# Kernel optimization log

Hardware: AMD Instinct MI355X
Metric: run time of the kernel (lower is better)

Reference implementation:

```python
import jax, jax.numpy as jnp
import numpy as np

B, M, NT, V, D, H, E, S = 4, 12, 12, 10000, 64, 3, 512, 32


def setup_inputs() -> dict:
    key = jax.random.key(0)
    ks = jax.random.split(key, 16)
    def rn(k, shape, scale=0.05):
        return jax.random.normal(k, shape, dtype=jnp.float32) * scale
    return {
        "tendency": jax.random.normal(ks[0], (B, M, V), dtype=jnp.float32),
        "periodicity": jax.random.normal(ks[1], (B, NT, V), dtype=jnp.float32),
        "edges": jax.random.randint(ks[2], (H, E, S), 0, V),
        "w1": rn(ks[3], (1, D)), "b1": rn(ks[4], (D,)),
        "w2": rn(ks[5], (D, D)), "b2": rn(ks[6], (D,)),
        "attn_w": rn(ks[7], (D, D)), "attn_a": rn(ks[8], (2 * D, 1)),
        "w_ih": rn(ks[9], (4 * D, D)), "w_hh": rn(ks[10], (4 * D, D)),
        "b_ih": rn(ks[11], (4 * D,)), "b_hh": rn(ks[12], (4 * D,)),
        "w_out": rn(ks[13], (2 * D, 1)), "b_out": rn(ks[14], (1,)),
    }


def _hypersage(X, edges, w, b):
    # X: (N, V, F); edges: (E, S) node indices. All edges have size S <= Q,
    # so torch's random subsampling is the identity.
    n, v, f = X.shape
    e, s = edges.shape
    gathered = X[:, edges, :]                      # (N, E, S, F)
    agg = gathered.mean(axis=2)                    # (N, E, F)
    flat = edges.reshape(-1)                       # (E*S,)
    contrib = jnp.broadcast_to(agg[:, :, None, :], (n, e, s, f)).reshape(n, e * s, f)
    X_out = jnp.zeros((n, v, f), X.dtype).at[:, flat, :].add(contrib)
    deg = jnp.zeros((v,), X.dtype).at[flat].add(1.0)
    deg = jnp.maximum(deg, 1.0)
    X_out = X_out / deg[None, :, None]
    return X_out @ w + b                           # Linear fc


def _attention(Xs, attn_w, attn_a):
    # Xs: (H, N, V, D)
    ref = Xs.mean(axis=0)                          # (N, V, D)
    wx = Xs @ attn_w                               # (H, N, V, D)
    wr = ref @ attn_w                              # (N, V, D)
    z = jnp.concatenate([wx, jnp.broadcast_to(wr[None], wx.shape)], axis=-1) @ attn_a
    z = jax.nn.leaky_relu(z, negative_slope=0.2)   # (H, N, V, 1)
    alpha = jax.nn.softmax(z, axis=0)
    return (alpha * Xs).sum(axis=0)                # (N, V, D)


def _lstm_final(x, w_ih, w_hh, b_ih, b_hh):
    # x: (BV, T, D) -> final hidden state (BV, D). PyTorch gate order i,f,g,o.
    bv, t, d = x.shape
    xg = x @ w_ih.T + (b_ih + b_hh)                # precompute input gates (BV, T, 4D)
    def step(carry, xg_t):
        h, c = carry
        g = xg_t + h @ w_hh.T
        i, f, gg, o = jnp.split(g, 4, axis=-1)
        c = jax.nn.sigmoid(f) * c + jax.nn.sigmoid(i) * jnp.tanh(gg)
        h = jax.nn.sigmoid(o) * jnp.tanh(c)
        return (h, c), None
    h0 = jnp.zeros((bv, d), x.dtype)
    (h, _), _ = jax.lax.scan(step, (h0, h0), jnp.swapaxes(xg, 0, 1))
    return h


def _branch(seq, edges, w1, b1, w2, b2, attn_w, attn_a, w_ih, w_hh, b_ih, b_hh):
    b, t, v = seq.shape
    X = seq.reshape(b * t, v, 1)                   # fold time into batch (same DAMHG per step)
    def per_hg(e):
        return _hypersage(_hypersage(X, e, w1, b1), e, w2, b2)
    xs = jax.vmap(per_hg)(edges)                   # (H, B*T, V, D)
    fused = _attention(xs, attn_w, attn_a)         # (B*T, V, D)
    d = fused.shape[-1]
    seq_v = fused.reshape(b, t, v, d).transpose(0, 2, 1, 3).reshape(b * v, t, d)
    h = _lstm_final(seq_v, w_ih, w_hh, b_ih, b_hh)
    return h.reshape(b, v, d)


def reference(tendency, periodicity, edges, w1, b1, w2, b2, attn_w, attn_a, w_ih, w_hh, b_ih, b_hh, w_out, b_out):
    h_t = _branch(tendency, edges, w1, b1, w2, b2, attn_w, attn_a, w_ih, w_hh, b_ih, b_hh)
    h_p = _branch(periodicity, edges, w1, b1, w2, b2, attn_w, attn_a, w_ih, w_hh, b_ih, b_hh)
    fusion = jnp.concatenate([h_t, h_p], axis=-1)  # (B, V, 2D)
    out = fusion @ w_out + b_out                   # (B, V, 1)
    return out[..., 0]
```

## Files before the change

kernel.cpp:

```cpp
#include <hip/hip_runtime.h>

#define NV 10000
#define NB 4
#define NTT 12
#define NSEQ 48
#define NH 3
#define NE 512
#define NS 32
#define ND 64

#define S_U   0
#define S_C1  64
#define S_V1  128
#define S_V2  192
#define S_SC  256
#define S_GU  272
#define S_GC  528
#define S_G0  784
#define F_INV 1040
#define F_M   (F_INV + NH*NV)
#define F_PQ  (F_M + NH*NV)
#define F_HT  (F_PQ + 4*NV*NSEQ)
#define I_CNT (F_HT + 2*NB*NV)
#define I_CUR (I_CNT + NH*NV)
#define I_OFF (I_CUR + NH*NV)
#define I_SLOT (I_OFF + NH*NV)
#define F_DYN (I_SLOT + NH*NE*NS)
#define XT_SZ  (NV*NSEQ)
#define AGG_SZ (NH*NE*NSEQ)
#define YZ_SZ  (NH*NV*NSEQ)

#define NZERO (2*NH*NV + NB*NV)

typedef __attribute__((ext_vector_type(8))) _Float16 f16x8;
typedef __attribute__((ext_vector_type(4))) float f32x4;

__device__ __forceinline__ unsigned short f2h(float x) {
  union { _Float16 h; unsigned short u; } c;
  c.h = (_Float16)x;
  return c.u;
}
__device__ __forceinline__ f16x8 ldsH(const unsigned short* p) {
  union { uint4 u; f16x8 v; } x;
  x.u = *(const uint4*)p;
  return x.v;
}

__global__ void k_init(const float* __restrict__ w1, const float* __restrict__ b1,
                       const float* __restrict__ w2, const float* __restrict__ b2,
                       const float* __restrict__ attn_w, const float* __restrict__ attn_a,
                       const float* __restrict__ w_ih, const float* __restrict__ b_ih,
                       const float* __restrict__ b_hh, float* __restrict__ ws,
                       int* __restrict__ cnt, float* __restrict__ out) {
  const int tid = threadIdx.x;
  if (blockIdx.x != 0) {
    const int g = (blockIdx.x - 1) * 256 + tid;
    if (g < 2 * NH * NV) cnt[g] = 0;
    else if (g < NZERO) out[g - 2 * NH * NV] = 0.0f;
    return;
  }
  __shared__ float u_s[64], c1_s[64];
  if (tid < 64) {
    float v1 = 0.f, v2 = 0.f, u = 0.f, c1 = 0.f;
    for (int d = 0; d < 64; ++d) {
      const float aw = attn_w[tid * 64 + d];
      v1 += aw * attn_a[d];
      v2 += aw * attn_a[64 + d];
      const float w2v = w2[d * 64 + tid];
      u  += w1[d] * w2v;
      c1 += b1[d] * w2v;
    }
    ws[S_U + tid] = u;  ws[S_C1 + tid] = c1;
    ws[S_V1 + tid] = v1; ws[S_V2 + tid] = v2;
    u_s[tid] = u; c1_s[tid] = c1;
  }
  __syncthreads();
  if (tid == 0) {
    float al = 0.f, be = 0.f, ga = 0.f, de = 0.f, ep = 0.f;
    for (int d = 0; d < 64; ++d) {
      const float v1 = ws[S_V1 + d], v2 = ws[S_V2 + d];
      al += u_s[d] * v1;  be += c1_s[d] * v1;
      ga += u_s[d] * v2;  de += c1_s[d] * v2;
      ep += b2[d] * (v1 + v2);
    }
    ws[S_SC + 0] = al; ws[S_SC + 1] = be; ws[S_SC + 2] = ga;
    ws[S_SC + 3] = de; ws[S_SC + 4] = ep;
  }
  {
    const int j = tid;
    float gu = 0.f, gc = 0.f, g0 = 0.f;
    for (int d = 0; d < 64; ++d) {
      const float w = w_ih[j * 64 + d];
      gu += w * u_s[d]; gc += w * c1_s[d]; g0 += w * b2[d];
    }
    ws[S_GU + j] = gu; ws[S_GC + j] = gc;
    ws[S_G0 + j] = g0 + b_ih[j] + b_hh[j];
  }
}

__global__ void k_count(const int* __restrict__ edges, int* __restrict__ counts) {
  const int g = blockIdx.x * 256 + threadIdx.x;
  if (g >= NH * NE * NS) return;
  const int h = g >> 14;
  atomicAdd(&counts[h * NV + edges[g]], 1);
}

__global__ void k_scan(const int* __restrict__ counts, int* __restrict__ offs,
                       float* __restrict__ invdeg, float* __restrict__ mvec) {
  const int h = blockIdx.x;
  const int tid = threadIdx.x;
  const int base = h * NV;
  const int CH = 10;
  int local[10];
  int run = 0;
  for (int i = 0; i < CH; ++i) {
    const int v = tid * CH + i;
    const int c = (v < NV) ? counts[base + v] : 0;
    local[i] = run; run += c;
  }
  __shared__ int sd[1024];
  sd[tid] = run;
  __syncthreads();
  int acc = run;
  for (int off = 1; off < 1024; off <<= 1) {
    const int t = (tid >= off) ? sd[tid - off] : 0;
    __syncthreads();
    acc += t; sd[tid] = acc;
    __syncthreads();
  }
  const int excl = acc - run;
  for (int i = 0; i < CH; ++i) {
    const int v = tid * CH + i;
    if (v < NV) {
      offs[base + v] = excl + local[i];
      const int c = counts[base + v];
      invdeg[base + v] = 1.0f / (float)((c > 0) ? c : 1);
      mvec[base + v] = (c > 0) ? 1.0f : 0.0f;
    }
  }
}

__global__ void k_fill(const int* __restrict__ edges, const int* __restrict__ offs,
                       int* __restrict__ cursor, int* __restrict__ slot_edge) {
  const int g = blockIdx.x * 256 + threadIdx.x;
  if (g >= NH * NE * NS) return;
  const int h = g >> 14;
  const int e = (g >> 5) & (NE - 1);
  const int v = edges[g];
  const int pos = atomicAdd(&cursor[h * NV + v], 1);
  slot_edge[h * NE * NS + offs[h * NV + v] + pos] = e;
}

__global__ void k_trans2(const float* __restrict__ s0, const float* __restrict__ s1,
                         float* __restrict__ xT, int xtS) {
  __shared__ float tile[128][49];
  const float* seq = blockIdx.y ? s1 : s0;
  float* o = xT + (size_t)blockIdx.y * xtS;
  const int v0 = blockIdx.x * 128;
  const int tid = threadIdx.x;
  for (int i = tid; i < 128 * NSEQ; i += 256) {
    const int n = i / 128, vl = i % 128;
    const int v = v0 + vl;
    tile[vl][n] = (v < NV) ? seq[n * NV + v] : 0.0f;
  }
  __syncthreads();
  for (int i = tid; i < 128 * NSEQ; i += 256) {
    const int vl = i / NSEQ, n = i % NSEQ;
    const int v = v0 + vl;
    if (v < NV) o[v * NSEQ + n] = tile[vl][n];
  }
}

__global__ void k_eagg1(const int* __restrict__ edges, const float* __restrict__ xT,
                        int xtS, float* __restrict__ agg, int aggS) {
  const int g = blockIdx.x * 256 + threadIdx.x;
  if (g >= NH * NE * 12) return;
  const float* x = xT + (size_t)blockIdx.y * xtS;
  float* a = agg + (size_t)blockIdx.y * aggS;
  const int n0 = (g % 12) * 4;
  const int e = (g / 12) % NE;
  const int h = g / (12 * NE);
  const int* ep = edges + (h * NE + e) * NS;
  float4 acc = make_float4(0.f, 0.f, 0.f, 0.f);
  for (int s = 0; s < NS; ++s) {
    const float4 t = *(const float4*)&x[ep[s] * NSEQ + n0];
    acc.x += t.x; acc.y += t.y; acc.z += t.z; acc.w += t.w;
  }
  acc.x *= (1.0f / NS); acc.y *= (1.0f / NS); acc.z *= (1.0f / NS); acc.w *= (1.0f / NS);
  *(float4*)&a[(h * NE + e) * NSEQ + n0] = acc;
}

__global__ void k_eagg2(const int* __restrict__ edges, const float* __restrict__ ysum,
                        int yS, const float* __restrict__ invdeg,
                        float* __restrict__ agg, int aggS) {
  const int g = blockIdx.x * 256 + threadIdx.x;
  if (g >= NH * NE * 12) return;
  const float* y = ysum + (size_t)blockIdx.y * yS;
  float* a = agg + (size_t)blockIdx.y * aggS;
  const int n0 = (g % 12) * 4;
  const int e = (g / 12) % NE;
  const int h = g / (12 * NE);
  const int* ep = edges + (h * NE + e) * NS;
  float4 acc = make_float4(0.f, 0.f, 0.f, 0.f);
  for (int s = 0; s < NS; ++s) {
    const int v = ep[s];
    const float iv = invdeg[h * NV + v];
    const float4 t = *(const float4*)&y[(h * NV + v) * NSEQ + n0];
    acc.x += t.x * iv; acc.y += t.y * iv; acc.z += t.z * iv; acc.w += t.w * iv;
  }
  acc.x *= (1.0f / NS); acc.y *= (1.0f / NS); acc.z *= (1.0f / NS); acc.w *= (1.0f / NS);
  *(float4*)&a[(h * NE + e) * NSEQ + n0] = acc;
}

__global__ void k_vg(const int* __restrict__ counts, const int* __restrict__ offs,
                     const int* __restrict__ slot_edge, const float* __restrict__ agg,
                     int aggS, float* __restrict__ outv, int outS) {
  const int g = blockIdx.x * 256 + threadIdx.x;
  if (g >= NH * NV * 12) return;
  const float* a = agg + (size_t)blockIdx.y * aggS;
  float* o = outv + (size_t)blockIdx.y * outS;
  const int n0 = (g % 12) * 4;
  const int v = (g / 12) % NV;
  const int h = g / (12 * NV);
  const int beg = offs[h * NV + v];
  const int cnt = counts[h * NV + v];
  const int* se = slot_edge + h * NE * NS;
  float4 acc = make_float4(0.f, 0.f, 0.f, 0.f);
  for (int i = 0; i < cnt; ++i) {
    const int e = se[beg + i];
    const float4 t = *(const float4*)&a[(h * NE + e) * NSEQ + n0];
    acc.x += t.x; acc.y += t.y; acc.z += t.z; acc.w += t.w;
  }
  *(float4*)&o[(h * NV + v) * NSEQ + n0] = acc;
}

__global__ void k_vgattn(const int* __restrict__ counts, const int* __restrict__ offs,
                         const int* __restrict__ slot_edge, const float* __restrict__ agg,
                         int aggS, const float* __restrict__ invdeg,
                         const float* __restrict__ mvec, const float* __restrict__ ws,
                         unsigned int* __restrict__ pq, int br0) {
  const int g = blockIdx.x * 256 + threadIdx.x;
  if (g >= NV * 12) return;
  const int bi = blockIdx.y;
  const float* a = agg + (size_t)bi * aggS;
  unsigned int* pbuf = pq + (size_t)(bi + br0) * NV * NSEQ;
  const int n0 = (g % 12) * 4;
  const int v = g / 12;
  const float al = ws[S_SC + 0], be = ws[S_SC + 1], ga = ws[S_SC + 2],
              de = ws[S_SC + 3], ep = ws[S_SC + 4];
  union { float4 v4; float f[4]; } zh[3];
  float mh[3];
  #pragma unroll
  for (int h = 0; h < NH; ++h) {
    const int beg = offs[h * NV + v];
    const int cnt = counts[h * NV + v];
    const int* se = slot_edge + h * NE * NS;
    float4 acc = make_float4(0.f, 0.f, 0.f, 0.f);
    for (int i = 0; i < cnt; ++i) {
      const int e = se[beg + i];
      const float4 t = *(const float4*)&a[(h * NE + e) * NSEQ + n0];
      acc.x += t.x; acc.y += t.y; acc.z += t.z; acc.w += t.w;
    }
    const float iv = invdeg[h * NV + v];
    zh[h].v4 = make_float4(acc.x * iv, acc.y * iv, acc.z * iv, acc.w * iv);
    mh[h] = mvec[h * NV + v];
  }
  const float mb = (mh[0] + mh[1] + mh[2]) * (1.f / 3.f);
  uint4 o4;
  unsigned int* op = (unsigned int*)&o4;
  #pragma unroll
  for (int j = 0; j < 4; ++j) {
    const float z0 = zh[0].f[j], z1 = zh[1].f[j], z2 = zh[2].f[j];
    const float zb = (z0 + z1 + z2) * (1.f / 3.f);
    float sc[3];
    const float zt[3] = {z0, z1, z2};
    #pragma unroll
    for (int h = 0; h < NH; ++h) {
      const float s = al * zt[h] + be * mh[h] + ga * zb + de * mb + ep;
      sc[h] = (s > 0.f) ? s : 0.2f * s;
    }
    const float mx = fmaxf(sc[0], fmaxf(sc[1], sc[2]));
    const float e0 = __expf(sc[0] - mx), e1 = __expf(sc[1] - mx), e2 = __expf(sc[2] - mx);
    const float inv = 1.0f / (e0 + e1 + e2);
    const float pv = (e0 * z0 + e1 * z1 + e2 * z2) * inv;
    const float qv = (e0 * mh[0] + e1 * mh[1] + e2 * mh[2]) * inv;
    op[j] = (unsigned int)f2h(pv) | ((unsigned int)f2h(qv) << 16);
  }
  *(uint4*)&pbuf[v * NSEQ + n0] = o4;
}

#define RS2 72
__launch_bounds__(256, 4)
__global__ void k_lstm2(const float* __restrict__ w_hh, const float* __restrict__ ws,
                        const unsigned int* __restrict__ pqbase,
                        const float* __restrict__ w_out, const float* __restrict__ b_out,
                        float* __restrict__ out) {
  __shared__ __align__(16) unsigned short smem[2 * 64 * RS2];
  __shared__ unsigned int pq_sh[NTT][64];
  const int tid = threadIdx.x;
  const int w = tid >> 6, lane = tid & 63, q = lane >> 4, l15 = lane & 15;
  const int b = blockIdx.y, br = blockIdx.z;
  const int v0 = blockIdx.x * 64;
  const int d = w * 16 + l15;

  union HU { uint4 u; f16x8 v; };

  const unsigned int* pqb = pqbase + (size_t)br * NV * NSEQ;
  if (tid < 192) {
    const int s = tid / 3, f4 = tid % 3;
    const int v = v0 + s;
    uint4 val = make_uint4(0u, 0u, 0u, 0u);
    if (v < NV) val = *(const uint4*)&pqb[v * NSEQ + b * NTT + f4 * 4];
    pq_sh[f4 * 4 + 0][s] = val.x; pq_sh[f4 * 4 + 1][s] = val.y;
    pq_sh[f4 * 4 + 2][s] = val.z; pq_sh[f4 * 4 + 3][s] = val.w;
  }

  f16x8 Bf[4][2];
  #pragma unroll
  for (int g = 0; g < 4; ++g)
    #pragma unroll
    for (int kh = 0; kh < 2; ++kh) {
      const float* wp = w_hh + (g * 64 + d) * 64 + kh * 32 + q * 8;
      const float4 lo = *(const float4*)wp;
      const float4 hi = *(const float4*)(wp + 4);
      HU f;
      f.u.x = (unsigned int)f2h(lo.x) | ((unsigned int)f2h(lo.y) << 16);
      f.u.y = (unsigned int)f2h(lo.z) | ((unsigned int)f2h(lo.w) << 16);
      f.u.z = (unsigned int)f2h(hi.x) | ((unsigned int)f2h(hi.y) << 16);
      f.u.w = (unsigned int)f2h(hi.z) | ((unsigned int)f2h(hi.w) << 16);
      Bf[g][kh] = f.v;
    }

  HU bex[4];
  #pragma unroll
  for (int g = 0; g < 4; ++g) {
    const float gu = ws[S_GU + g * 64 + d];
    const float gc = ws[S_GC + g * 64 + d];
    const float g0 = ws[S_G0 + g * 64 + d];
    bex[g].u.x = (q == 0) ? ((unsigned int)f2h(gu) | ((unsigned int)f2h(gc) << 16)) : 0u;
    bex[g].u.y = (q == 0) ? (unsigned int)f2h(g0) : 0u;
    bex[g].u.z = 0u; bex[g].u.w = 0u;
  }
  const float WO = w_out[br * 64 + d];
  const float BO = b_out[0];
  __syncthreads();

  f32x4 cst[4];
  float pr[4][4];
  #pragma unroll
  for (int mi = 0; mi < 4; ++mi) cst[mi] = (f32x4){0.f, 0.f, 0.f, 0.f};
  const f32x4 z4 = (f32x4){0.f, 0.f, 0.f, 0.f};

  #pragma unroll 1
  for (int t = 0; t < NTT; ++t) {
    const unsigned short* hr = smem + ((t + 1) & 1) * (64 * RS2);
    unsigned short* hw = smem + (t & 1) * (64 * RS2);
    const bool last = (t == NTT - 1);
    #pragma unroll
    for (int mi = 0; mi < 4; ++mi) {
      HU ae;
      ae.u.x = (q == 0) ? pq_sh[t][mi * 16 + l15] : 0u;
      ae.u.y = (q == 0) ? 0x3C00u : 0u;
      ae.u.z = 0u; ae.u.w = 0u;
      f32x4 aI = __builtin_amdgcn_mfma_f32_16x16x32_f16(ae.v, bex[0].v, z4, 0, 0, 0);
      f32x4 aF = __builtin_amdgcn_mfma_f32_16x16x32_f16(ae.v, bex[1].v, z4, 0, 0, 0);
      f32x4 aG = __builtin_amdgcn_mfma_f32_16x16x32_f16(ae.v, bex[2].v, z4, 0, 0, 0);
      f32x4 aO = __builtin_amdgcn_mfma_f32_16x16x32_f16(ae.v, bex[3].v, z4, 0, 0, 0);
      if (t > 0) {
        #pragma unroll
        for (int kh = 0; kh < 2; ++kh) {
          const f16x8 Ah = ldsH(&hr[(mi * 16 + l15) * RS2 + kh * 32 + q * 8]);
          aI = __builtin_amdgcn_mfma_f32_16x16x32_f16(Ah, Bf[0][kh], aI, 0, 0, 0);
          aF = __builtin_amdgcn_mfma_f32_16x16x32_f16(Ah, Bf[1][kh], aF, 0, 0, 0);
          aG = __builtin_amdgcn_mfma_f32_16x16x32_f16(Ah, Bf[2][kh], aG, 0, 0, 0);
          aO = __builtin_amdgcn_mfma_f32_16x16x32_f16(Ah, Bf[3][kh], aO, 0, 0, 0);
        }
      }
      #pragma unroll
      for (int r = 0; r < 4; ++r) {
        const float c  = cst[mi][r];
        const float ea = __expf(-aI[r]);
        const float eb = __expf(-2.0f * aG[r]);
        const float ef = __expf(-aF[r]);
        const float A  = 1.0f + ea, Bb = 1.0f + eb, Fd = 1.0f + ef;
        const float P  = A * Bb;
        const float numer = fmaf(c, P, (1.0f - eb) * Fd);
        const float cn = numer * __builtin_amdgcn_rcpf(Fd * P);
        cst[mi][r] = cn;
        const float ec = __expf(-aO[r]);
        const float ed = __expf(-2.0f * cn);
        const float h = (1.0f - ed) *
            __builtin_amdgcn_rcpf((1.0f + ec) * (1.0f + ed));
        if (!last) {
          hw[(mi * 16 + q * 4 + r) * RS2 + d] = f2h(h);
        } else {
          pr[mi][r] = h * WO;
        }
      }
    }
    __syncthreads();
  }
  float* fbuf = (float*)smem;
  #pragma unroll
  for (int mi = 0; mi < 4; ++mi)
    #pragma unroll
    for (int r = 0; r < 4; ++r) {
      float v = pr[mi][r];
      v += __shfl_xor(v, 1);
      v += __shfl_xor(v, 2);
      v += __shfl_xor(v, 4);
      v += __shfl_xor(v, 8);
      if (l15 == 0) fbuf[w * 64 + mi * 16 + q * 4 + r] = v;
    }
  __syncthreads();
  if (tid < 64) {
    const int v = v0 + tid;
    if (v < NV) {
      const float s = fbuf[tid] + fbuf[64 + tid] + fbuf[128 + tid] + fbuf[192 + tid];
      atomicAdd(&out[b * NV + v], s + ((br == 0) ? BO : 0.0f));
    }
  }
}

extern "C" void kernel_launch(void* const* d_in, const int* in_sizes, int n_in,
                              void* d_out, int out_size, void* d_ws, size_t ws_size,
                              hipStream_t stream) {
  const float* tend   = (const float*)d_in[0];
  const float* peri   = (const float*)d_in[1];
  const int*   edges  = (const int*)d_in[2];
  const float* w1     = (const float*)d_in[3];
  const float* b1     = (const float*)d_in[4];
  const float* w2     = (const float*)d_in[5];
  const float* b2     = (const float*)d_in[6];
  const float* attn_w = (const float*)d_in[7];
  const float* attn_a = (const float*)d_in[8];
  const float* w_ih   = (const float*)d_in[9];
  const float* w_hh   = (const float*)d_in[10];
  const float* b_ih   = (const float*)d_in[11];
  const float* b_hh   = (const float*)d_in[12];
  const float* w_out  = (const float*)d_in[13];
  const float* b_out  = (const float*)d_in[14];
  float* out = (float*)d_out;
  float* ws  = (float*)d_ws;
  int*   iws = (int*)d_ws;
  int* cnt = iws + I_CNT;
  int* cur = iws + I_CUR;
  int* off = iws + I_OFF;
  int* sed = iws + I_SLOT;
  unsigned int* pqw = (unsigned int*)(ws + F_PQ);

  const size_t need2 = ((size_t)F_DYN + 2 * (XT_SZ + AGG_SZ + YZ_SZ)) * 4;
  const bool batched = ws_size >= need2;
  const int nb = batched ? 2 : 1;
  float* XT  = ws + F_DYN;
  float* AGG = XT + (size_t)nb * XT_SZ;
  float* YZ  = AGG + (size_t)nb * AGG_SZ;

  k_init<<<1 + (NZERO + 255) / 256, 256, 0, stream>>>(
      w1, b1, w2, b2, attn_w, attn_a, w_ih, b_ih, b_hh, ws, cnt, out);
  k_count<<<(NH * NE * NS) / 256, 256, 0, stream>>>(edges, cnt);
  k_scan<<<NH, 1024, 0, stream>>>(cnt, off, ws + F_INV, ws + F_M);
  k_fill<<<(NH * NE * NS) / 256, 256, 0, stream>>>(edges, off, cur, sed);

  const int g_eagg = (NH * NE * 12 + 255) / 256;
  const int g_vg   = (NH * NV * 12 + 255) / 256;
  const int g_attn = (NV * 12 + 255) / 256;
  if (batched) {
    k_trans2<<<dim3((NV + 127) / 128, 2), 256, 0, stream>>>(tend, peri, XT, XT_SZ);
    k_eagg1<<<dim3(g_eagg, 2), 256, 0, stream>>>(edges, XT, XT_SZ, AGG, AGG_SZ);
    k_vg<<<dim3(g_vg, 2), 256, 0, stream>>>(cnt, off, sed, AGG, AGG_SZ, YZ, YZ_SZ);
    k_eagg2<<<dim3(g_eagg, 2), 256, 0, stream>>>(edges, YZ, YZ_SZ, ws + F_INV, AGG, AGG_SZ);
    k_vgattn<<<dim3(g_attn, 2), 256, 0, stream>>>(cnt, off, sed, AGG, AGG_SZ,
                                                  ws + F_INV, ws + F_M, ws, pqw, 0);
  } else {
    for (int br = 0; br < 2; ++br) {
      const float* seq = br ? peri : tend;
      k_trans2<<<dim3((NV + 127) / 128, 1), 256, 0, stream>>>(seq, seq, XT, 0);
      k_eagg1<<<dim3(g_eagg, 1), 256, 0, stream>>>(edges, XT, 0, AGG, 0);
      k_vg<<<dim3(g_vg, 1), 256, 0, stream>>>(cnt, off, sed, AGG, 0, YZ, 0);
      k_eagg2<<<dim3(g_eagg, 1), 256, 0, stream>>>(edges, YZ, 0, ws + F_INV, AGG, 0);
      k_vgattn<<<dim3(g_attn, 1), 256, 0, stream>>>(cnt, off, sed, AGG, 0,
                                                    ws + F_INV, ws + F_M, ws, pqw, br);
    }
  }
  dim3 lgrid((NV + 63) / 64, NB, 2);
  k_lstm2<<<lgrid, 256, 0, stream>>>(w_hh, ws, pqw, w_out, b_out, out);
}
```

Measured before the change: 242.9 us.

## Split edge aggregation across 8 lanes and halve LSTM vertex tile

The edge-aggregation kernels now spread each edge's 32 members across 8 lanes, each summing 4 gathered rows, and combine the partial sums with shuffle-xor reductions. This launches 8x more threads and exposes more memory-level parallelism for the scattered gathers. The LSTM kernel now processes 32 vertices per block instead of 64 on a flattened 1D grid, doubling block count to raise occupancy and cut tail effects. In exchange, each LSTM block loads its converted w_hh weights for half as many vertices, and half the MFMA tiles per wave are gone, so per-block fixed overhead grows.

New measurement: 238.1 us. -2.0%, faster.

```diff
diff --git a/kernel.cpp b/kernel.cpp
--- a/kernel.cpp
+++ b/kernel.cpp
@@ -8,6 +8,7 @@
 #define NE 512
 #define NS 32
 #define ND 64
+#define NVT 313
 
 #define S_U   0
 #define S_C1  64
@@ -174,42 +175,66 @@
 __global__ void k_eagg1(const int* __restrict__ edges, const float* __restrict__ xT,
                         int xtS, float* __restrict__ agg, int aggS) {
   const int g = blockIdx.x * 256 + threadIdx.x;
-  if (g >= NH * NE * 12) return;
+  if (g >= NH * NE * 12 * 8) return;
   const float* x = xT + (size_t)blockIdx.y * xtS;
   float* a = agg + (size_t)blockIdx.y * aggS;
-  const int n0 = (g % 12) * 4;
-  const int e = (g / 12) % NE;
-  const int h = g / (12 * NE);
-  const int* ep = edges + (h * NE + e) * NS;
+  const int sub = g & 7;
+  const int o = g >> 3;
+  const int n0 = (o % 12) * 4;
+  const int e = (o / 12) % NE;
+  const int h = o / (12 * NE);
+  const int* ep = edges + (h * NE + e) * NS + sub * 4;
   float4 acc = make_float4(0.f, 0.f, 0.f, 0.f);
-  for (int s = 0; s < NS; ++s) {
+  #pragma unroll
+  for (int s = 0; s < 4; ++s) {
     const float4 t = *(const float4*)&x[ep[s] * NSEQ + n0];
     acc.x += t.x; acc.y += t.y; acc.z += t.z; acc.w += t.w;
   }
-  acc.x *= (1.0f / NS); acc.y *= (1.0f / NS); acc.z *= (1.0f / NS); acc.w *= (1.0f / NS);
-  *(float4*)&a[(h * NE + e) * NSEQ + n0] = acc;
+  #pragma unroll
+  for (int m = 1; m < 8; m <<= 1) {
+    acc.x += __shfl_xor(acc.x, m);
+    acc.y += __shfl_xor(acc.y, m);
+    acc.z += __shfl_xor(acc.z, m);
+    acc.w += __shfl_xor(acc.w, m);
+  }
+  if (sub == 0) {
+    acc.x *= (1.0f / NS); acc.y *= (1.0f / NS); acc.z *= (1.0f / NS); acc.w *= (1.0f / NS);
+    *(float4*)&a[(h * NE + e) * NSEQ + n0] = acc;
+  }
 }
 
 __global__ void k_eagg2(const int* __restrict__ edges, const float* __restrict__ ysum,
                         int yS, const float* __restrict__ invdeg,
                         float* __restrict__ agg, int aggS) {
   const int g = blockIdx.x * 256 + threadIdx.x;
-  if (g >= NH * NE * 12) return;
+  if (g >= NH * NE * 12 * 8) return;
   const float* y = ysum + (size_t)blockIdx.y * yS;
   float* a = agg + (size_t)blockIdx.y * aggS;
-  const int n0 = (g % 12) * 4;
-  const int e = (g / 12) % NE;
-  const int h = g / (12 * NE);
-  const int* ep = edges + (h * NE + e) * NS;
+  const int sub = g & 7;
+  const int o = g >> 3;
+  const int n0 = (o % 12) * 4;
+  const int e = (o / 12) % NE;
+  const int h = o / (12 * NE);
+  const int* ep = edges + (h * NE + e) * NS + sub * 4;
   float4 acc = make_float4(0.f, 0.f, 0.f, 0.f);
-  for (int s = 0; s < NS; ++s) {
+  #pragma unroll
+  for (int s = 0; s < 4; ++s) {
     const int v = ep[s];
     const float iv = invdeg[h * NV + v];
     const float4 t = *(const float4*)&y[(h * NV + v) * NSEQ + n0];
     acc.x += t.x * iv; acc.y += t.y * iv; acc.z += t.z * iv; acc.w += t.w * iv;
   }
-  acc.x *= (1.0f / NS); acc.y *= (1.0f / NS); acc.z *= (1.0f / NS); acc.w *= (1.0f / NS);
-  *(float4*)&a[(h * NE + e) * NSEQ + n0] = acc;
+  #pragma unroll
+  for (int m = 1; m < 8; m <<= 1) {
+    acc.x += __shfl_xor(acc.x, m);
+    acc.y += __shfl_xor(acc.y, m);
+    acc.z += __shfl_xor(acc.z, m);
+    acc.w += __shfl_xor(acc.w, m);
+  }
+  if (sub == 0) {
+    acc.x *= (1.0f / NS); acc.y *= (1.0f / NS); acc.z *= (1.0f / NS); acc.w *= (1.0f / NS);
+    *(float4*)&a[(h * NE + e) * NSEQ + n0] = acc;
+  }
 }
 
 __global__ void k_vg(const int* __restrict__ counts, const int* __restrict__ offs,
@@ -295,18 +320,21 @@
                         const unsigned int* __restrict__ pqbase,
                         const float* __restrict__ w_out, const float* __restrict__ b_out,
                         float* __restrict__ out) {
-  __shared__ __align__(16) unsigned short smem[2 * 64 * RS2];
-  __shared__ unsigned int pq_sh[NTT][64];
+  __shared__ __align__(16) unsigned short smem[2 * 32 * RS2];
+  __shared__ unsigned int pq_sh[NTT][32];
   const int tid = threadIdx.x;
   const int w = tid >> 6, lane = tid & 63, q = lane >> 4, l15 = lane & 15;
-  const int b = blockIdx.y, br = blockIdx.z;
-  const int v0 = blockIdx.x * 64;
+  const int bid = blockIdx.x;
+  const int vt = bid % NVT;
+  const int b  = (bid / NVT) % NB;
+  const int br = bid / (NVT * NB);
+  const int v0 = vt * 32;
   const int d = w * 16 + l15;
 
   union HU { uint4 u; f16x8 v; };
 
   const unsigned int* pqb = pqbase + (size_t)br * NV * NSEQ;
-  if (tid < 192) {
+  if (tid < 96) {
     const int s = tid / 3, f4 = tid % 3;
     const int v = v0 + s;
     uint4 val = make_uint4(0u, 0u, 0u, 0u);
@@ -345,19 +373,19 @@
   const float BO = b_out[0];
   __syncthreads();
 
-  f32x4 cst[4];
-  float pr[4][4];
-  #pragma unroll
-  for (int mi = 0; mi < 4; ++mi) cst[mi] = (f32x4){0.f, 0.f, 0.f, 0.f};
+  f32x4 cst[2];
+  float pr[2][4];
+  #pragma unroll
+  for (int mi = 0; mi < 2; ++mi) cst[mi] = (f32x4){0.f, 0.f, 0.f, 0.f};
   const f32x4 z4 = (f32x4){0.f, 0.f, 0.f, 0.f};
 
   #pragma unroll 1
   for (int t = 0; t < NTT; ++t) {
-    const unsigned short* hr = smem + ((t + 1) & 1) * (64 * RS2);
-    unsigned short* hw = smem + (t & 1) * (64 * RS2);
+    const unsigned short* hr = smem + ((t + 1) & 1) * (32 * RS2);
+    unsigned short* hw = smem + (t & 1) * (32 * RS2);
     const bool last = (t == NTT - 1);
     #pragma unroll
-    for (int mi = 0; mi < 4; ++mi) {
+    for (int mi = 0; mi < 2; ++mi) {
       HU ae;
       ae.u.x = (q == 0) ? pq_sh[t][mi * 16 + l15] : 0u;
       ae.u.y = (q == 0) ? 0x3C00u : 0u;
@@ -402,7 +430,7 @@
   }
   float* fbuf = (float*)smem;
   #pragma unroll
-  for (int mi = 0; mi < 4; ++mi)
+  for (int mi = 0; mi < 2; ++mi)
     #pragma unroll
     for (int r = 0; r < 4; ++r) {
       float v = pr[mi][r];
@@ -410,13 +438,13 @@
       v += __shfl_xor(v, 2);
       v += __shfl_xor(v, 4);
       v += __shfl_xor(v, 8);
-      if (l15 == 0) fbuf[w * 64 + mi * 16 + q * 4 + r] = v;
+      if (l15 == 0) fbuf[w * 32 + mi * 16 + q * 4 + r] = v;
     }
   __syncthreads();
-  if (tid < 64) {
+  if (tid < 32) {
     const int v = v0 + tid;
     if (v < NV) {
-      const float s = fbuf[tid] + fbuf[64 + tid] + fbuf[128 + tid] + fbuf[192 + tid];
+      const float s = fbuf[tid] + fbuf[32 + tid] + fbuf[64 + tid] + fbuf[96 + tid];
       atomicAdd(&out[b * NV + v], s + ((br == 0) ? BO : 0.0f));
     }
   }
@@ -462,7 +490,7 @@
   k_scan<<<NH, 1024, 0, stream>>>(cnt, off, ws + F_INV, ws + F_M);
   k_fill<<<(NH * NE * NS) / 256, 256, 0, stream>>>(edges, off, cur, sed);
 
-  const int g_eagg = (NH * NE * 12 + 255) / 256;
+  const int g_eagg = (NH * NE * 12 * 8) / 256;
   const int g_vg   = (NH * NV * 12 + 255) / 256;
   const int g_attn = (NV * 12 + 255) / 256;
   if (batched) {
@@ -483,6 +511,5 @@
                                                     ws + F_INV, ws + F_M, ws, pqw, br);
     }
   }
-  dim3 lgrid((NV + 63) / 64, NB, 2);
-  k_lstm2<<<lgrid, 256, 0, stream>>>(w_hh, ws, pqw, w_out, b_out, out);
-}
+  k_lstm2<<<NVT * NB * 2, 256, 0, stream>>>(w_hh, ws, pqw, w_out, b_out, out);
+}
```
